# Optimization experiments

Measured on AMD Instinct MI355X. Metric: run time of the kernel, lower is better.

## Reference

```python
import jax, jax.numpy as jnp
import numpy as np

N = 128
NPTS = 120000
G = 64  # voxel grid side


def _build_coords_and_nbrs():
    rng = np.random.default_rng(0)
    lin = rng.choice(G ** 3, size=NPTS, replace=False)
    xs = lin // (G * G)
    ys = (lin // G) % G
    zs = lin % G
    lut = np.full(G ** 3, -1, np.int32)
    lut[lin] = np.arange(NPTS, dtype=np.int32)
    nbr = np.full((NPTS, 27), -1, np.int32)
    k = 0
    for dx in (-1, 0, 1):
        for dy in (-1, 0, 1):
            for dz in (-1, 0, 1):
                nx, ny, nz = xs + dx, ys + dy, zs + dz
                ok = (nx >= 0) & (nx < G) & (ny >= 0) & (ny < G) & (nz >= 0) & (nz < G)
                nl = np.clip(nx * G * G + ny * G + nz, 0, G ** 3 - 1)
                nbr[:, k] = np.where(ok, lut[nl], -1)
                k += 1
    return nbr


def setup_inputs() -> dict:
    key = jax.random.key(0)
    k = jax.random.split(key, 6)
    H = N // 2
    x = jax.random.normal(k[0], (NPTS, N), jnp.float32)
    W1s = jax.random.normal(k[1], (6, N, H), jnp.float32) * np.sqrt(2.0 / N)
    Wks = jax.random.normal(k[2], (6, 27, H, H), jnp.float32) * np.sqrt(2.0 / (27 * H))
    W2s = jax.random.normal(k[3], (6, H, N), jnp.float32) * np.sqrt(1.0 / H)
    Wf = jax.random.normal(k[4], (N, N), jnp.float32) * np.sqrt(1.0 / N)
    nbr_idx = jnp.asarray(_build_coords_and_nbrs())
    return {"x": x, "W1s": W1s, "Wks": Wks, "W2s": W2s, "Wf": Wf, "nbr_idx": nbr_idx}


def reference(x, W1s, Wks, W2s, Wf, nbr_idx):
    valid = nbr_idx >= 0                      # [NPTS, 27]
    safe = jnp.maximum(nbr_idx, 0)

    def conv3(h, Wk):
        # gather-matmul-scatter over the 27 coordinate offsets (as ME does)
        out = jnp.zeros((h.shape[0], Wk.shape[2]), h.dtype)
        for kk in range(27):
            g = jnp.where(valid[:, kk, None], h[safe[:, kk]], 0.0)
            out = out + g @ Wk[kk]
        return out

    def residual_unit(h, i):
        t = jax.nn.relu(h @ W1s[i])           # 1x1 conv N -> N/2
        t = jax.nn.relu(conv3(t, Wks[i]))     # 3^3 sparse conv N/2 -> N/2
        t = t @ W2s[i]                        # 1x1 conv N/2 -> N
        return jax.nn.relu(t + h)

    a = x
    for i in range(3):
        a = residual_unit(a, i)
    b = x
    for i in range(3, 6):
        b = residual_unit(b, i)
    b = b @ Wf                                # final 1x1 conv in branch b
    return a * jax.nn.sigmoid(b) + x
```

## Files before the change

### kernel.cpp

```cpp
#include <hip/hip_runtime.h>
#include <stdint.h>

#define NPTS 120000

typedef __attribute__((ext_vector_type(8))) short bf16x8;
typedef __attribute__((ext_vector_type(4))) float f32x4;

__device__ __forceinline__ uint16_t f2b(float f) {
    union { float f; uint32_t i; } v; v.f = f;
    uint32_t x = v.i;
    return (uint16_t)((x + 0x7fffu + ((x >> 16) & 1u)) >> 16);
}
__device__ __forceinline__ float b2f(uint16_t u) {
    union { uint32_t i; float f; } v; v.i = ((uint32_t)u) << 16; return v.f;
}
__device__ __forceinline__ bf16x8 cvt8(f32x4 a, f32x4 b) {
    bf16x8 t;
    t[0] = (short)f2b(a[0]); t[1] = (short)f2b(a[1]);
    t[2] = (short)f2b(a[2]); t[3] = (short)f2b(a[3]);
    t[4] = (short)f2b(b[0]); t[5] = (short)f2b(b[1]);
    t[6] = (short)f2b(b[2]); t[7] = (short)f2b(b[3]);
    return t;
}
#define MFMA(a, b, c) __builtin_amdgcn_mfma_f32_16x16x32_bf16((a), (b), (c), 0, 0, 0)

__global__ __launch_bounds__(256) void k_swz(
    const float* __restrict__ W1s, const float* __restrict__ Wks,
    const float* __restrict__ W2s, const float* __restrict__ Wf,
    uint16_t* __restrict__ Z, uint16_t* __restrict__ T1z,
    uint16_t* __restrict__ T2z)
{
    if (blockIdx.x == 0) {
        if (threadIdx.x < 64)
            T1z[(size_t)NPTS * 64 + threadIdx.x] = 0;
        else if (threadIdx.x < 128 && T2z)
            T2z[(size_t)NPTS * 64 + (threadIdx.x - 64)] = 0;
    }
    int idx = blockIdx.x * 256 + threadIdx.x;
    if (idx >= 778240) return;
    const float* src; int K, N, r;
    if (idx < 49152)       { src = W1s + (idx / 8192) * 8192;           K = 128; N = 64;  r = idx & 8191; }
    else if (idx < 712704) { int t = idx - 49152;  src = Wks + (t >> 12) * 4096; K = 64;  N = 64;  r = t & 4095; }
    else if (idx < 761856) { int t = idx - 712704; src = W2s + (t / 8192) * 8192; K = 64;  N = 128; r = t & 8191; }
    else                   { src = Wf; K = 128; N = 128; r = idx - 761856; }
    int j  = r & 7;
    int l  = (r >> 3) & 63;
    int t2 = r >> 9;
    int KC = K >> 5;
    int kc = t2 % KC;
    int nt = t2 / KC;
    int k  = kc * 32 + (l >> 4) * 8 + j;
    int n  = nt * 16 + (l & 15);
    Z[idx] = f2b(src[k * N + n]);
}

__global__ __launch_bounds__(256) void k_nbrT(
    const int* __restrict__ nbr, int* __restrict__ nbrT)
{
    __shared__ int st[27 * 64];
    const int tid = threadIdx.x;
    const long p0 = (long)blockIdx.x * 64;
    for (int i = tid; i < 1728; i += 256) {
        int lp = i / 27, kk = i - lp * 27;
        int n = nbr[p0 * 27 + i];
        st[kk * 64 + lp] = ((n < 0) ? NPTS : n) << 6;
    }
    __syncthreads();
    for (int i = tid; i < 1728; i += 256) {
        int kk = i >> 6, lp = i & 63;
        nbrT[(long)kk * NPTS + p0 + lp] = st[i];
    }
}

__device__ __forceinline__ void gemm1_body(
    int b, const float* __restrict__ H, const uint16_t* __restrict__ Wz,
    uint16_t* __restrict__ T)
{
    const int tid = threadIdx.x;
    const int wv = tid >> 6, ln = tid & 63;
    const int m = ln & 15, part = ln >> 4;
    const long rb = (long)b * 64 + wv * 16;

    bf16x8 a[4];
    const float* hrow = H + (rb + m) * 128 + part * 8;
    #pragma unroll
    for (int kc = 0; kc < 4; ++kc) {
        f32x4 h0 = *reinterpret_cast<const f32x4*>(hrow + kc * 32);
        f32x4 h1 = *reinterpret_cast<const f32x4*>(hrow + kc * 32 + 4);
        a[kc] = cvt8(h0, h1);
    }
    #pragma unroll
    for (int nt = 0; nt < 4; ++nt) {
        f32x4 acc = (f32x4)(0.0f);
        #pragma unroll
        for (int kc = 0; kc < 4; ++kc) {
            bf16x8 b8 = *reinterpret_cast<const bf16x8*>(Wz + ((nt * 4 + kc) * 64 + ln) * 8);
            acc = MFMA(a[kc], b8, acc);
        }
        #pragma unroll
        for (int r = 0; r < 4; ++r) {
            float v = acc[r] > 0.f ? acc[r] : 0.f;
            T[(rb + part * 4 + r) * 64 + nt * 16 + m] = f2b(v);
        }
    }
}

__global__ __launch_bounds__(256) void k_gemm1(
    const float* __restrict__ H, const uint16_t* __restrict__ Wz,
    uint16_t* __restrict__ T)
{
    gemm1_body(blockIdx.x, H, Wz, T);
}

__global__ __launch_bounds__(256) void k_gemm1p(
    const float* __restrict__ HA, const float* __restrict__ HB,
    const uint16_t* __restrict__ WzA, const uint16_t* __restrict__ WzB,
    uint16_t* __restrict__ TA, uint16_t* __restrict__ TB)
{
    int b = blockIdx.x;
    if (b < 1875) gemm1_body(b, HA, WzA, TA);
    else          gemm1_body(b - 1875, HB, WzB, TB);
}

struct SM {
    uint16_t wkbuf[2][4096];
    uint16_t uni[4][3456];
};

__device__ __forceinline__ void gather6(bf16x8 (&dst)[3][2], const int (&ix)[3],
                                        const uint16_t* __restrict__ T, int pc8)
{
    #pragma unroll
    for (int mm = 0; mm < 3; ++mm) {
        const uint16_t* s = T + (long)ix[mm] + pc8;
        dst[mm][0] = *reinterpret_cast<const bf16x8*>(s);
        dst[mm][1] = *reinterpret_cast<const bf16x8*>(s + 32);
    }
}
__device__ __forceinline__ void ldidx(int (&ix)[3], const int* __restrict__ p, int mrow)
{
    #pragma unroll
    for (int mm = 0; mm < 3; ++mm) ix[mm] = p[mm * 16 + mrow];
}
__device__ __forceinline__ void pload(bf16x8& s0, bf16x8& s1, const uint16_t* __restrict__ g)
{
    s0 = *reinterpret_cast<const bf16x8*>(g);
    s1 = *reinterpret_cast<const bf16x8*>(g + 512);
}
__device__ __forceinline__ void tap24(f32x4 (&acc)[3][4], const bf16x8 (&A)[3][2],
                                      const uint16_t* wk, int ln)
{
    bf16x8 B[8];
    #pragma unroll
    for (int i = 0; i < 8; ++i)
        B[i] = *reinterpret_cast<const bf16x8*>(wk + i * 512 + ln * 8);
    #pragma unroll
    for (int nt = 0; nt < 4; ++nt)
        #pragma unroll
        for (int mm = 0; mm < 3; ++mm) {
            acc[mm][nt] = MFMA(A[mm][0], B[nt * 2 + 0], acc[mm][nt]);
            acc[mm][nt] = MFMA(A[mm][1], B[nt * 2 + 1], acc[mm][nt]);
        }
}

template<int MODE>
__device__ __forceinline__ void conv_body(
    SM& sm, int blk,
    const uint16_t* __restrict__ T, const uint16_t* __restrict__ Wkz,
    const uint16_t* __restrict__ W2z, const float* Hin,
    const int* __restrict__ nbrT, float* HoutF, uint16_t* __restrict__ HoutB)
{
    const int tid = threadIdx.x;
    const int wv = tid >> 6, ln = tid & 63;
    const int mrow = ln & 15, part = ln >> 4, pc8 = part * 8;
    const long bb = (long)blk * 192;
    const long wb0 = bb + wv * 48;

    {
        bf16x8 s0, s1;
        pload(s0, s1, Wkz + wv * 1024 + ln * 8);
        *reinterpret_cast<bf16x8*>(&sm.wkbuf[0][wv * 1024 + ln * 8]) = s0;
        *reinterpret_cast<bf16x8*>(&sm.wkbuf[0][wv * 1024 + 512 + ln * 8]) = s1;
    }
    int ixA[3], ixB[3];
    bf16x8 pA[3][2], pB[3][2];
    ldidx(ixA, nbrT + wb0, mrow);
    gather6(pA, ixA, T, pc8);
    ldidx(ixB, nbrT + (long)NPTS + wb0, mrow);

    f32x4 acc[3][4];
    #pragma unroll
    for (int mm = 0; mm < 3; ++mm)
        #pragma unroll
        for (int nt = 0; nt < 4; ++nt) acc[mm][nt] = (f32x4)(0.0f);
    __syncthreads();

    #pragma unroll 1
    for (int t = 0; t < 26; t += 2) {
        bf16x8 s0, s1;
        gather6(pB, ixB, T, pc8);
        pload(s0, s1, Wkz + (t + 1) * 4096 + wv * 1024 + ln * 8);
        if (t + 2 < 27) ldidx(ixA, nbrT + (long)(t + 2) * NPTS + wb0, mrow);
        tap24(acc, pA, &sm.wkbuf[0][0], ln);
        *reinterpret_cast<bf16x8*>(&sm.wkbuf[1][wv * 1024 + ln * 8]) = s0;
        *reinterpret_cast<bf16x8*>(&sm.wkbuf[1][wv * 1024 + 512 + ln * 8]) = s1;
        __syncthreads();
        if (t + 1 < 26) {
            gather6(pA, ixA, T, pc8);
            pload(s0, s1, Wkz + (t + 2) * 4096 + wv * 1024 + ln * 8);
            if (t + 3 < 27) ldidx(ixB, nbrT + (long)(t + 3) * NPTS + wb0, mrow);
        }
        tap24(acc, pB, &sm.wkbuf[1][0], ln);
        if (t + 1 < 26) {
            *reinterpret_cast<bf16x8*>(&sm.wkbuf[0][wv * 1024 + ln * 8]) = s0;
            *reinterpret_cast<bf16x8*>(&sm.wkbuf[0][wv * 1024 + 512 + ln * 8]) = s1;
        }
        __syncthreads();
    }
    tap24(acc, pA, &sm.wkbuf[0][0], ln);

    uint16_t* sc2 = &sm.uni[wv][0];
    #pragma unroll
    for (int mm = 0; mm < 3; ++mm)
        #pragma unroll
        for (int nt = 0; nt < 4; ++nt)
            #pragma unroll
            for (int r = 0; r < 4; ++r) {
                float v = acc[mm][nt][r];
                v = v > 0.f ? v : 0.f;
                sc2[(mm * 16 + part * 4 + r) * 72 + nt * 16 + mrow] = f2b(v);
            }
    __builtin_amdgcn_wave_barrier();

    bf16x8 a2[3][2];
    #pragma unroll
    for (int mm = 0; mm < 3; ++mm) {
        const uint16_t* crow = sc2 + (mm * 16 + mrow) * 72;
        a2[mm][0] = *reinterpret_cast<const bf16x8*>(crow + pc8);
        a2[mm][1] = *reinterpret_cast<const bf16x8*>(crow + 32 + pc8);
    }
    __builtin_amdgcn_wave_barrier();

    #pragma unroll 2
    for (int nt = 0; nt < 8; ++nt) {
        bf16x8 b0 = *reinterpret_cast<const bf16x8*>(W2z + ((nt * 2 + 0) * 64 + ln) * 8);
        bf16x8 b1 = *reinterpret_cast<const bf16x8*>(W2z + ((nt * 2 + 1) * 64 + ln) * 8);
        f32x4 c[3];
        #pragma unroll
        for (int mm = 0; mm < 3; ++mm) {
            c[mm] = (f32x4)(0.0f);
            c[mm] = MFMA(a2[mm][0], b0, c[mm]);
            c[mm] = MFMA(a2[mm][1], b1, c[mm]);
        }
        const int col = nt * 16 + mrow;
        if (MODE == 0) {
            #pragma unroll
            for (int mm = 0; mm < 3; ++mm)
                #pragma unroll
                for (int r = 0; r < 4; ++r) {
                    long p = wb0 + mm * 16 + part * 4 + r;
                    float v = c[mm][r] + Hin[p * 128 + col];
                    HoutF[p * 128 + col] = v > 0.f ? v : 0.f;
                }
        } else {
            #pragma unroll
            for (int mm = 0; mm < 3; ++mm)
                #pragma unroll
                for (int r = 0; r < 4; ++r) {
                    long p = wb0 + mm * 16 + part * 4 + r;
                    float v = c[mm][r] + Hin[p * 128 + col];
                    v = v > 0.f ? v : 0.f;
                    HoutB[p * 128 + col] = f2b(v);
                }
        }
    }
}

template<int MODE>
__global__ __launch_bounds__(256, 3) void k_conv1(
    const uint16_t* __restrict__ T, const uint16_t* __restrict__ Wkz,
    const uint16_t* __restrict__ W2z, const float* Hin,
    const int* __restrict__ nbrT, float* HoutF, uint16_t* __restrict__ HoutB)
{
    __shared__ SM sm;
    conv_body<MODE>(sm, blockIdx.x, T, Wkz, W2z, Hin, nbrT, HoutF, HoutB);
}

template<int MA, int MB>
__global__ __launch_bounds__(256, 3) void k_convp(
    const uint16_t* __restrict__ Ta, const uint16_t* __restrict__ Tb,
    const uint16_t* __restrict__ WkzA, const uint16_t* __restrict__ WkzB,
    const uint16_t* __restrict__ W2zA, const uint16_t* __restrict__ W2zB,
    const float* HinA, const float* HinB,
    const int* __restrict__ nbrT,
    float* HoFA, float* HoFB,
    uint16_t* __restrict__ HoBA, uint16_t* __restrict__ HoBB)
{
    __shared__ SM sm;
    int b = blockIdx.x;
    if (b < 625) conv_body<MA>(sm, b, Ta, WkzA, W2zA, HinA, nbrT, HoFA, HoBA);
    else         conv_body<MB>(sm, b - 625, Tb, WkzB, W2zB, HinB, nbrT, HoFB, HoBB);
}

__global__ __launch_bounds__(256) void k_final(
    const float* B, const uint16_t* __restrict__ Wfz,
    const uint16_t* __restrict__ A16, const float* __restrict__ X,
    float* Out)
{
    const int tid = threadIdx.x;
    const int wv = tid >> 6, ln = tid & 63;
    const int m = ln & 15, part = ln >> 4;
    const long rb = (long)blockIdx.x * 64 + wv * 16;

    bf16x8 a[4];
    const float* brow = B + (rb + m) * 128 + part * 8;
    #pragma unroll
    for (int kc = 0; kc < 4; ++kc) {
        f32x4 h0 = *reinterpret_cast<const f32x4*>(brow + kc * 32);
        f32x4 h1 = *reinterpret_cast<const f32x4*>(brow + kc * 32 + 4);
        a[kc] = cvt8(h0, h1);
    }
    #pragma unroll
    for (int nt = 0; nt < 8; ++nt) {
        f32x4 acc = (f32x4)(0.0f);
        #pragma unroll
        for (int kc = 0; kc < 4; ++kc) {
            bf16x8 b = *reinterpret_cast<const bf16x8*>(Wfz + ((nt * 4 + kc) * 64 + ln) * 8);
            acc = MFMA(a[kc], b, acc);
        }
        #pragma unroll
        for (int r = 0; r < 4; ++r) {
            long p = rb + part * 4 + r;
            int col = nt * 16 + m;
            float s = 1.f / (1.f + __expf(-acc[r]));
            float av = b2f(A16[p * 128 + col]);
            Out[p * 128 + col] = av * s + X[p * 128 + col];
        }
    }
}

extern "C" void kernel_launch(void* const* d_in, const int* in_sizes, int n_in,
                              void* d_out, int out_size, void* d_ws, size_t ws_size,
                              hipStream_t stream)
{
    const float* x   = (const float*)d_in[0];
    const float* W1s = (const float*)d_in[1];
    const float* Wks = (const float*)d_in[2];
    const float* W2s = (const float*)d_in[3];
    const float* Wf  = (const float*)d_in[4];
    const int*   nbr = (const int*)d_in[5];
    float*       out = (float*)d_out;

    const size_t A16_sh = (size_t)NPTS * 128;
    const size_t T_sh   = (size_t)(NPTS + 1) * 64;
    const size_t Z_sh   = 778240;
    const size_t nbrT_i = (size_t)27 * NPTS;

    uint16_t* A16 = (uint16_t*)d_ws;
    uint16_t* Ta  = A16 + A16_sh;
    uint16_t* Tb  = Ta + T_sh;
    uint16_t* Z   = Tb + T_sh;
    int* nbrT     = (int*)(Z + Z_sh);
    float* Ha     = (float*)(nbrT + nbrT_i);
    size_t need_paired = (size_t)((char*)(Ha + A16_sh) - (char*)d_ws);

    if (ws_size >= need_paired) {
        const uint16_t* W1z = Z;
        const uint16_t* Wkz = Z + 49152;
        const uint16_t* W2z = Z + 712704;
        const uint16_t* Wfz = Z + 761856;

        k_swz <<<dim3(3040), dim3(256), 0, stream>>>(W1s, Wks, W2s, Wf, Z, Ta, Tb);
        k_nbrT<<<dim3(1875), dim3(256), 0, stream>>>(nbr, nbrT);

        k_gemm1p<<<dim3(3750), dim3(256), 0, stream>>>(x, x, W1z, W1z + 3 * 8192, Ta, Tb);
        k_convp<0, 0><<<dim3(1250), dim3(256), 0, stream>>>(
            Ta, Tb, Wkz + 0 * 110592, Wkz + 3 * 110592, W2z + 0 * 8192, W2z + 3 * 8192,
            x, x, nbrT, Ha, out, nullptr, nullptr);
        k_gemm1p<<<dim3(3750), dim3(256), 0, stream>>>(Ha, out, W1z + 1 * 8192, W1z + 4 * 8192, Ta, Tb);
        k_convp<0, 0><<<dim3(1250), dim3(256), 0, stream>>>(
            Ta, Tb, Wkz + 1 * 110592, Wkz + 4 * 110592, W2z + 1 * 8192, W2z + 4 * 8192,
            Ha, out, nbrT, Ha, out, nullptr, nullptr);
        k_gemm1p<<<dim3(3750), dim3(256), 0, stream>>>(Ha, out, W1z + 2 * 8192, W1z + 5 * 8192, Ta, Tb);
        k_convp<1, 0><<<dim3(1250), dim3(256), 0, stream>>>(
            Ta, Tb, Wkz + 2 * 110592, Wkz + 5 * 110592, W2z + 2 * 8192, W2z + 5 * 8192,
            Ha, out, nbrT, nullptr, out, A16, nullptr);
        k_final<<<dim3(1875), dim3(256), 0, stream>>>(out, Wfz, A16, x, out);
    } else {
        uint16_t* Zs   = Ta + T_sh;
        int* nbrTs     = (int*)(Zs + Z_sh);
        const uint16_t* W1z = Zs;
        const uint16_t* Wkz = Zs + 49152;
        const uint16_t* W2z = Zs + 712704;
        const uint16_t* Wfz = Zs + 761856;

        k_swz <<<dim3(3040), dim3(256), 0, stream>>>(W1s, Wks, W2s, Wf, Zs, Ta, nullptr);
        k_nbrT<<<dim3(1875), dim3(256), 0, stream>>>(nbr, nbrTs);

        auto g1 = [&](int i, const float* h) {
            k_gemm1<<<dim3(1875), dim3(256), 0, stream>>>(h, W1z + (size_t)i * 8192, Ta);
        };
        g1(0, x);
        k_conv1<0><<<dim3(625), dim3(256), 0, stream>>>(Ta, Wkz + 0 * 110592, W2z + 0 * 8192, x,   nbrTs, out, nullptr);
        g1(1, out);
        k_conv1<0><<<dim3(625), dim3(256), 0, stream>>>(Ta, Wkz + 1 * 110592, W2z + 1 * 8192, out, nbrTs, out, nullptr);
        g1(2, out);
        k_conv1<1><<<dim3(625), dim3(256), 0, stream>>>(Ta, Wkz + 2 * 110592, W2z + 2 * 8192, out, nbrTs, nullptr, A16);
        g1(3, x);
        k_conv1<0><<<dim3(625), dim3(256), 0, stream>>>(Ta, Wkz + 3 * 110592, W2z + 3 * 8192, x,   nbrTs, out, nullptr);
        g1(4, out);
        k_conv1<0><<<dim3(625), dim3(256), 0, stream>>>(Ta, Wkz + 4 * 110592, W2z + 4 * 8192, out, nbrTs, out, nullptr);
        g1(5, out);
        k_conv1<0><<<dim3(625), dim3(256), 0, stream>>>(Ta, Wkz + 5 * 110592, W2z + 5 * 8192, out, nbrTs, out, nullptr);
        k_final<<<dim3(1875), dim3(256), 0, stream>>>(out, Wfz, A16, x, out);
    }
}
```

Measured before the change: 666.8 us.

## Use single-wave conv blocks reading tap weights directly from global memory

```diff
diff --git a/kernel.cpp b/kernel.cpp
--- a/kernel.cpp
+++ b/kernel.cpp
@@ -122,11 +122,6 @@
     else          gemm1_body(b - 1875, HB, WzB, TB);
 }
 
-struct SM {
-    uint16_t wkbuf[2][4096];
-    uint16_t uni[4][3456];
-};
-
 __device__ __forceinline__ void gather6(bf16x8 (&dst)[3][2], const int (&ix)[3],
                                         const uint16_t* __restrict__ T, int pc8)
 {
@@ -142,18 +137,13 @@
     #pragma unroll
     for (int mm = 0; mm < 3; ++mm) ix[mm] = p[mm * 16 + mrow];
 }
-__device__ __forceinline__ void pload(bf16x8& s0, bf16x8& s1, const uint16_t* __restrict__ g)
-{
-    s0 = *reinterpret_cast<const bf16x8*>(g);
-    s1 = *reinterpret_cast<const bf16x8*>(g + 512);
-}
-__device__ __forceinline__ void tap24(f32x4 (&acc)[3][4], const bf16x8 (&A)[3][2],
-                                      const uint16_t* wk, int ln)
+__device__ __forceinline__ void tap24g(f32x4 (&acc)[3][4], const bf16x8 (&A)[3][2],
+                                       const uint16_t* __restrict__ wk, int ln)
 {
     bf16x8 B[8];
     #pragma unroll
     for (int i = 0; i < 8; ++i)
-        B[i] = *reinterpret_cast<const bf16x8*>(wk + i * 512 + ln * 8);
+        B[i] = *reinterpret_cast<const bf16x8*>(wk + (i * 64 + ln) * 8);
     #pragma unroll
     for (int nt = 0; nt < 4; ++nt)
         #pragma unroll
@@ -164,24 +154,16 @@
 }
 
 template<int MODE>
-__device__ __forceinline__ void conv_body(
-    SM& sm, int blk,
+__device__ __forceinline__ void conv_body1(
+    uint16_t* sc2, int blk,
     const uint16_t* __restrict__ T, const uint16_t* __restrict__ Wkz,
     const uint16_t* __restrict__ W2z, const float* Hin,
     const int* __restrict__ nbrT, float* HoutF, uint16_t* __restrict__ HoutB)
 {
-    const int tid = threadIdx.x;
-    const int wv = tid >> 6, ln = tid & 63;
+    const int ln = threadIdx.x & 63;
     const int mrow = ln & 15, part = ln >> 4, pc8 = part * 8;
-    const long bb = (long)blk * 192;
-    const long wb0 = bb + wv * 48;
-
-    {
-        bf16x8 s0, s1;
-        pload(s0, s1, Wkz + wv * 1024 + ln * 8);
-        *reinterpret_cast<bf16x8*>(&sm.wkbuf[0][wv * 1024 + ln * 8]) = s0;
-        *reinterpret_cast<bf16x8*>(&sm.wkbuf[0][wv * 1024 + 512 + ln * 8]) = s1;
-    }
+    const long wb0 = (long)blk * 48;
+
     int ixA[3], ixB[3];
     bf16x8 pA[3][2], pB[3][2];
     ldidx(ixA, nbrT + wb0, mrow);
@@ -193,33 +175,20 @@
     for (int mm = 0; mm < 3; ++mm)
         #pragma unroll
         for (int nt = 0; nt < 4; ++nt) acc[mm][nt] = (f32x4)(0.0f);
-    __syncthreads();
 
     #pragma unroll 1
     for (int t = 0; t < 26; t += 2) {
-        bf16x8 s0, s1;
         gather6(pB, ixB, T, pc8);
-        pload(s0, s1, Wkz + (t + 1) * 4096 + wv * 1024 + ln * 8);
         if (t + 2 < 27) ldidx(ixA, nbrT + (long)(t + 2) * NPTS + wb0, mrow);
-        tap24(acc, pA, &sm.wkbuf[0][0], ln);
-        *reinterpret_cast<bf16x8*>(&sm.wkbuf[1][wv * 1024 + ln * 8]) = s0;
-        *reinterpret_cast<bf16x8*>(&sm.wkbuf[1][wv * 1024 + 512 + ln * 8]) = s1;
-        __syncthreads();
+        tap24g(acc, pA, Wkz + t * 4096, ln);
         if (t + 1 < 26) {
             gather6(pA, ixA, T, pc8);
-            pload(s0, s1, Wkz + (t + 2) * 4096 + wv * 1024 + ln * 8);
             if (t + 3 < 27) ldidx(ixB, nbrT + (long)(t + 3) * NPTS + wb0, mrow);
         }
-        tap24(acc, pB, &sm.wkbuf[1][0], ln);
-        if (t + 1 < 26) {
-            *reinterpret_cast<bf16x8*>(&sm.wkbuf[0][wv * 1024 + ln * 8]) = s0;
-            *reinterpret_cast<bf16x8*>(&sm.wkbuf[0][wv * 1024 + 512 + ln * 8]) = s1;
-        }
-        __syncthreads();
-    }
-    tap24(acc, pA, &sm.wkbuf[0][0], ln);
-
-    uint16_t* sc2 = &sm.uni[wv][0];
+        tap24g(acc, pB, Wkz + (t + 1) * 4096, ln);
+    }
+    tap24g(acc, pA, Wkz + 26 * 4096, ln);
+
     #pragma unroll
     for (int mm = 0; mm < 3; ++mm)
         #pragma unroll
@@ -277,17 +246,17 @@
 }
 
 template<int MODE>
-__global__ __launch_bounds__(256, 3) void k_conv1(
+__global__ __launch_bounds__(64, 4) void k_conv1(
     const uint16_t* __restrict__ T, const uint16_t* __restrict__ Wkz,
     const uint16_t* __restrict__ W2z, const float* Hin,
     const int* __restrict__ nbrT, float* HoutF, uint16_t* __restrict__ HoutB)
 {
-    __shared__ SM sm;
-    conv_body<MODE>(sm, blockIdx.x, T, Wkz, W2z, Hin, nbrT, HoutF, HoutB);
+    __shared__ uint16_t sc2[48 * 72];
+    conv_body1<MODE>(sc2, blockIdx.x, T, Wkz, W2z, Hin, nbrT, HoutF, HoutB);
 }
 
 template<int MA, int MB>
-__global__ __launch_bounds__(256, 3) void k_convp(
+__global__ __launch_bounds__(64, 4) void k_convp1(
     const uint16_t* __restrict__ Ta, const uint16_t* __restrict__ Tb,
     const uint16_t* __restrict__ WkzA, const uint16_t* __restrict__ WkzB,
     const uint16_t* __restrict__ W2zA, const uint16_t* __restrict__ W2zB,
@@ -296,10 +265,10 @@
     float* HoFA, float* HoFB,
     uint16_t* __restrict__ HoBA, uint16_t* __restrict__ HoBB)
 {
-    __shared__ SM sm;
+    __shared__ uint16_t sc2[48 * 72];
     int b = blockIdx.x;
-    if (b < 625) conv_body<MA>(sm, b, Ta, WkzA, W2zA, HinA, nbrT, HoFA, HoBA);
-    else         conv_body<MB>(sm, b - 625, Tb, WkzB, W2zB, HinB, nbrT, HoFB, HoBB);
+    if (b < 2500) conv_body1<MA>(sc2, b, Ta, WkzA, W2zA, HinA, nbrT, HoFA, HoBA);
+    else          conv_body1<MB>(sc2, b - 2500, Tb, WkzB, W2zB, HinB, nbrT, HoFB, HoBB);
 }
 
 __global__ __launch_bounds__(256) void k_final(
@@ -374,15 +343,15 @@
         k_nbrT<<<dim3(1875), dim3(256), 0, stream>>>(nbr, nbrT);
 
         k_gemm1p<<<dim3(3750), dim3(256), 0, stream>>>(x, x, W1z, W1z + 3 * 8192, Ta, Tb);
-        k_convp<0, 0><<<dim3(1250), dim3(256), 0, stream>>>(
+        k_convp1<0, 0><<<dim3(5000), dim3(64), 0, stream>>>(
             Ta, Tb, Wkz + 0 * 110592, Wkz + 3 * 110592, W2z + 0 * 8192, W2z + 3 * 8192,
             x, x, nbrT, Ha, out, nullptr, nullptr);
         k_gemm1p<<<dim3(3750), dim3(256), 0, stream>>>(Ha, out, W1z + 1 * 8192, W1z + 4 * 8192, Ta, Tb);
-        k_convp<0, 0><<<dim3(1250), dim3(256), 0, stream>>>(
+        k_convp1<0, 0><<<dim3(5000), dim3(64), 0, stream>>>(
             Ta, Tb, Wkz + 1 * 110592, Wkz + 4 * 110592, W2z + 1 * 8192, W2z + 4 * 8192,
             Ha, out, nbrT, Ha, out, nullptr, nullptr);
         k_gemm1p<<<dim3(3750), dim3(256), 0, stream>>>(Ha, out, W1z + 2 * 8192, W1z + 5 * 8192, Ta, Tb);
-        k_convp<1, 0><<<dim3(1250), dim3(256), 0, stream>>>(
+        k_convp1<1, 0><<<dim3(5000), dim3(64), 0, stream>>>(
             Ta, Tb, Wkz + 2 * 110592, Wkz + 5 * 110592, W2z + 2 * 8192, W2z + 5 * 8192,
             Ha, out, nbrT, nullptr, out, A16, nullptr);
         k_final<<<dim3(1875), dim3(256), 0, stream>>>(out, Wfz, A16, x, out);
@@ -401,17 +370,17 @@
             k_gemm1<<<dim3(1875), dim3(256), 0, stream>>>(h, W1z + (size_t)i * 8192, Ta);
         };
         g1(0, x);
-        k_conv1<0><<<dim3(625), dim3(256), 0, stream>>>(Ta, Wkz + 0 * 110592, W2z + 0 * 8192, x,   nbrTs, out, nullptr);
+        k_conv1<0><<<dim3(2500), dim3(64), 0, stream>>>(Ta, Wkz + 0 * 110592, W2z + 0 * 8192, x,   nbrTs, out, nullptr);
         g1(1, out);
-        k_conv1<0><<<dim3(625), dim3(256), 0, stream>>>(Ta, Wkz + 1 * 110592, W2z + 1 * 8192, out, nbrTs, out, nullptr);
+        k_conv1<0><<<dim3(2500), dim3(64), 0, stream>>>(Ta, Wkz + 1 * 110592, W2z + 1 * 8192, out, nbrTs, out, nullptr);
         g1(2, out);
-        k_conv1<1><<<dim3(625), dim3(256), 0, stream>>>(Ta, Wkz + 2 * 110592, W2z + 2 * 8192, out, nbrTs, nullptr, A16);
+        k_conv1<1><<<dim3(2500), dim3(64), 0, stream>>>(Ta, Wkz + 2 * 110592, W2z + 2 * 8192, out, nbrTs, nullptr, A16);
         g1(3, x);
-        k_conv1<0><<<dim3(625), dim3(256), 0, stream>>>(Ta, Wkz + 3 * 110592, W2z + 3 * 8192, x,   nbrTs, out, nullptr);
+        k_conv1<0><<<dim3(2500), dim3(64), 0, stream>>>(Ta, Wkz + 3 * 110592, W2z + 3 * 8192, x,   nbrTs, out, nullptr);
         g1(4, out);
-        k_conv1<0><<<dim3(625), dim3(256), 0, stream>>>(Ta, Wkz + 4 * 110592, W2z + 4 * 8192, out, nbrTs, out, nullptr);
+        k_conv1<0><<<dim3(2500), dim3(64), 0, stream>>>(Ta, Wkz + 4 * 110592, W2z + 4 * 8192, out, nbrTs, out, nullptr);
         g1(5, out);
-        k_conv1<0><<<dim3(625), dim3(256), 0, stream>>>(Ta, Wkz + 5 * 110592, W2z + 5 * 8192, out, nbrTs, out, nullptr);
+        k_conv1<0><<<dim3(2500), dim3(64), 0, stream>>>(Ta, Wkz + 5 * 110592, W2z + 5 * 8192, out, nbrTs, out, nullptr);
         k_final<<<dim3(1875), dim3(256), 0, stream>>>(out, Wfz, A16, x, out);
     }
 }
```

Result: slower. 777.6 us (+16.6%).

## Stage MFMA epilogues through LDS for coalesced vector global stores

Applied to the files above, without the earlier changes.

```diff
diff --git a/kernel.cpp b/kernel.cpp
--- a/kernel.cpp
+++ b/kernel.cpp
@@ -5,6 +5,7 @@
 
 typedef __attribute__((ext_vector_type(8))) short bf16x8;
 typedef __attribute__((ext_vector_type(4))) float f32x4;
+typedef __attribute__((ext_vector_type(4))) unsigned short u16x4;
 
 __device__ __forceinline__ uint16_t f2b(float f) {
     union { float f; uint32_t i; } v; v.f = f;
@@ -73,13 +74,14 @@
 }
 
 __device__ __forceinline__ void gemm1_body(
-    int b, const float* __restrict__ H, const uint16_t* __restrict__ Wz,
-    uint16_t* __restrict__ T)
+    uint16_t* ts, int b, const float* __restrict__ H,
+    const uint16_t* __restrict__ Wz, uint16_t* __restrict__ T)
 {
     const int tid = threadIdx.x;
     const int wv = tid >> 6, ln = tid & 63;
     const int m = ln & 15, part = ln >> 4;
     const long rb = (long)b * 64 + wv * 16;
+    uint16_t* myts = ts + wv * 1024;
 
     bf16x8 a[4];
     const float* hrow = H + (rb + m) * 128 + part * 8;
@@ -100,8 +102,16 @@
         #pragma unroll
         for (int r = 0; r < 4; ++r) {
             float v = acc[r] > 0.f ? acc[r] : 0.f;
-            T[(rb + part * 4 + r) * 64 + nt * 16 + m] = f2b(v);
-        }
+            myts[(part * 4 + r) * 64 + nt * 16 + m] = f2b(v);
+        }
+    }
+    __builtin_amdgcn_wave_barrier();
+    #pragma unroll
+    for (int it = 0; it < 4; ++it) {
+        int idx = it * 256 + ln * 4;
+        int row = idx >> 6, col = idx & 63;
+        *reinterpret_cast<u16x4*>(&T[(rb + row) * 64 + col]) =
+            *reinterpret_cast<const u16x4*>(&myts[idx]);
     }
 }
 
@@ -109,7 +119,8 @@
     const float* __restrict__ H, const uint16_t* __restrict__ Wz,
     uint16_t* __restrict__ T)
 {
-    gemm1_body(blockIdx.x, H, Wz, T);
+    __shared__ uint16_t ts[4 * 1024];
+    gemm1_body(ts, blockIdx.x, H, Wz, T);
 }
 
 __global__ __launch_bounds__(256) void k_gemm1p(
@@ -117,15 +128,11 @@
     const uint16_t* __restrict__ WzA, const uint16_t* __restrict__ WzB,
     uint16_t* __restrict__ TA, uint16_t* __restrict__ TB)
 {
+    __shared__ uint16_t ts[4 * 1024];
     int b = blockIdx.x;
-    if (b < 1875) gemm1_body(b, HA, WzA, TA);
-    else          gemm1_body(b - 1875, HB, WzB, TB);
-}
-
-struct SM {
-    uint16_t wkbuf[2][4096];
-    uint16_t uni[4][3456];
-};
+    if (b < 1875) gemm1_body(ts, b, HA, WzA, TA);
+    else          gemm1_body(ts, b - 1875, HB, WzB, TB);
+}
 
 __device__ __forceinline__ void gather6(bf16x8 (&dst)[3][2], const int (&ix)[3],
                                         const uint16_t* __restrict__ T, int pc8)
@@ -165,7 +172,7 @@
 
 template<int MODE>
 __device__ __forceinline__ void conv_body(
-    SM& sm, int blk,
+    char* smem, int blk,
     const uint16_t* __restrict__ T, const uint16_t* __restrict__ Wkz,
     const uint16_t* __restrict__ W2z, const float* Hin,
     const int* __restrict__ nbrT, float* HoutF, uint16_t* __restrict__ HoutB)
@@ -176,11 +183,14 @@
     const long bb = (long)blk * 192;
     const long wb0 = bb + wv * 48;
 
+    uint16_t* wk0 = (uint16_t*)smem;
+    uint16_t* wk1 = (uint16_t*)(smem + 8192);
+
     {
         bf16x8 s0, s1;
         pload(s0, s1, Wkz + wv * 1024 + ln * 8);
-        *reinterpret_cast<bf16x8*>(&sm.wkbuf[0][wv * 1024 + ln * 8]) = s0;
-        *reinterpret_cast<bf16x8*>(&sm.wkbuf[0][wv * 1024 + 512 + ln * 8]) = s1;
+        *reinterpret_cast<bf16x8*>(&wk0[wv * 1024 + ln * 8]) = s0;
+        *reinterpret_cast<bf16x8*>(&wk0[wv * 1024 + 512 + ln * 8]) = s1;
     }
     int ixA[3], ixB[3];
     bf16x8 pA[3][2], pB[3][2];
@@ -201,25 +211,28 @@
         gather6(pB, ixB, T, pc8);
         pload(s0, s1, Wkz + (t + 1) * 4096 + wv * 1024 + ln * 8);
         if (t + 2 < 27) ldidx(ixA, nbrT + (long)(t + 2) * NPTS + wb0, mrow);
-        tap24(acc, pA, &sm.wkbuf[0][0], ln);
-        *reinterpret_cast<bf16x8*>(&sm.wkbuf[1][wv * 1024 + ln * 8]) = s0;
-        *reinterpret_cast<bf16x8*>(&sm.wkbuf[1][wv * 1024 + 512 + ln * 8]) = s1;
+        tap24(acc, pA, wk0, ln);
+        *reinterpret_cast<bf16x8*>(&wk1[wv * 1024 + ln * 8]) = s0;
+        *reinterpret_cast<bf16x8*>(&wk1[wv * 1024 + 512 + ln * 8]) = s1;
         __syncthreads();
         if (t + 1 < 26) {
             gather6(pA, ixA, T, pc8);
             pload(s0, s1, Wkz + (t + 2) * 4096 + wv * 1024 + ln * 8);
             if (t + 3 < 27) ldidx(ixB, nbrT + (long)(t + 3) * NPTS + wb0, mrow);
         }
-        tap24(acc, pB, &sm.wkbuf[1][0], ln);
+        tap24(acc, pB, wk1, ln);
         if (t + 1 < 26) {
-            *reinterpret_cast<bf16x8*>(&sm.wkbuf[0][wv * 1024 + ln * 8]) = s0;
-            *reinterpret_cast<bf16x8*>(&sm.wkbuf[0][wv * 1024 + 512 + ln * 8]) = s1;
+            *reinterpret_cast<bf16x8*>(&wk0[wv * 1024 + ln * 8]) = s0;
+            *reinterpret_cast<bf16x8*>(&wk0[wv * 1024 + 512 + ln * 8]) = s1;
         }
         __syncthreads();
     }
-    tap24(acc, pA, &sm.wkbuf[0][0], ln);
-
-    uint16_t* sc2 = &sm.uni[wv][0];
+    tap24(acc, pA, wk0, ln);
+    __syncthreads();
+
+    char* myr = smem + wv * 8192;
+    uint16_t* sc2 = (uint16_t*)myr;
+
     #pragma unroll
     for (int mm = 0; mm < 3; ++mm)
         #pragma unroll
@@ -241,53 +254,63 @@
     }
     __builtin_amdgcn_wave_barrier();
 
-    #pragma unroll 2
-    for (int nt = 0; nt < 8; ++nt) {
-        bf16x8 b0 = *reinterpret_cast<const bf16x8*>(W2z + ((nt * 2 + 0) * 64 + ln) * 8);
-        bf16x8 b1 = *reinterpret_cast<const bf16x8*>(W2z + ((nt * 2 + 1) * 64 + ln) * 8);
-        f32x4 c[3];
-        #pragma unroll
-        for (int mm = 0; mm < 3; ++mm) {
-            c[mm] = (f32x4)(0.0f);
-            c[mm] = MFMA(a2[mm][0], b0, c[mm]);
-            c[mm] = MFMA(a2[mm][1], b1, c[mm]);
-        }
-        const int col = nt * 16 + mrow;
-        if (MODE == 0) {
+    float* stg = (float*)myr;
+    #pragma unroll 1
+    for (int mm = 0; mm < 3; ++mm) {
+        #pragma unroll 2
+        for (int nt = 0; nt < 8; ++nt) {
+            bf16x8 b0 = *reinterpret_cast<const bf16x8*>(W2z + ((nt * 2 + 0) * 64 + ln) * 8);
+            bf16x8 b1 = *reinterpret_cast<const bf16x8*>(W2z + ((nt * 2 + 1) * 64 + ln) * 8);
+            f32x4 c = (f32x4)(0.0f);
+            c = MFMA(a2[mm][0], b0, c);
+            c = MFMA(a2[mm][1], b1, c);
             #pragma unroll
-            for (int mm = 0; mm < 3; ++mm)
+            for (int r = 0; r < 4; ++r)
+                stg[(part * 4 + r) * 128 + nt * 16 + mrow] = c[r];
+        }
+        __builtin_amdgcn_wave_barrier();
+        #pragma unroll
+        for (int it = 0; it < 8; ++it) {
+            int idx = it * 256 + ln * 4;
+            int row = idx >> 7, col = idx & 127;
+            long p = wb0 + mm * 16 + row;
+            f32x4 s = *reinterpret_cast<const f32x4*>(&stg[idx]);
+            f32x4 h = *reinterpret_cast<const f32x4*>(&Hin[p * 128 + col]);
+            if (MODE == 0) {
+                f32x4 o;
                 #pragma unroll
-                for (int r = 0; r < 4; ++r) {
-                    long p = wb0 + mm * 16 + part * 4 + r;
-                    float v = c[mm][r] + Hin[p * 128 + col];
-                    HoutF[p * 128 + col] = v > 0.f ? v : 0.f;
+                for (int q = 0; q < 4; ++q) {
+                    float v = s[q] + h[q];
+                    o[q] = v > 0.f ? v : 0.f;
                 }
-        } else {
-            #pragma unroll
-            for (int mm = 0; mm < 3; ++mm)
+                *reinterpret_cast<f32x4*>(&HoutF[p * 128 + col]) = o;
+            } else {
+                u16x4 o;
                 #pragma unroll
-                for (int r = 0; r < 4; ++r) {
-                    long p = wb0 + mm * 16 + part * 4 + r;
-                    float v = c[mm][r] + Hin[p * 128 + col];
+                for (int q = 0; q < 4; ++q) {
+                    float v = s[q] + h[q];
                     v = v > 0.f ? v : 0.f;
-                    HoutB[p * 128 + col] = f2b(v);
+                    o[q] = f2b(v);
                 }
-        }
+                *reinterpret_cast<u16x4*>(&HoutB[p * 128 + col]) = o;
+            }
+        }
+        __builtin_amdgcn_wave_barrier();
     }
 }
 
 template<int MODE>
-__global__ __launch_bounds__(256, 3) void k_conv1(
+__global__ __launch_bounds__(256, 5) void k_conv1(
     const uint16_t* __restrict__ T, const uint16_t* __restrict__ Wkz,
     const uint16_t* __restrict__ W2z, const float* Hin,
     const int* __restrict__ nbrT, float* HoutF, uint16_t* __restrict__ HoutB)
 {
-    __shared__ SM sm;
-    conv_body<MODE>(sm, blockIdx.x, T, Wkz, W2z, Hin, nbrT, HoutF, HoutB);
+    __shared__ __align__(16) char smem[32768];
+    conv_body<MODE>(smem, blockIdx.x, T, Wkz, W2z, Hin, nbrT, HoutF, HoutB);
 }
 
 template<int MA, int MB>
-__global__ __launch_bounds__(256, 3) void k_convp(
+__global__ __launch_bounds__(256, 5) void k_convp(
     const uint16_t* __restrict__ Ta, const uint16_t* __restrict__ Tb,
     const uint16_t* __restrict__ WkzA, const uint16_t* __restrict__ WkzB,
     const uint16_t* __restrict__ W2zA, const uint16_t* __restrict__ W2zB,
@@ -296,10 +319,10 @@
     float* HoFA, float* HoFB,
     uint16_t* __restrict__ HoBA, uint16_t* __restrict__ HoBB)
 {
-    __shared__ SM sm;
+    __shared__ __align__(16) char smem[32768];
     int b = blockIdx.x;
-    if (b < 625) conv_body<MA>(sm, b, Ta, WkzA, W2zA, HinA, nbrT, HoFA, HoBA);
-    else         conv_body<MB>(sm, b - 625, Tb, WkzB, W2zB, HinB, nbrT, HoFB, HoBB);
+    if (b < 625) conv_body<MA>(smem, b, Ta, WkzA, W2zA, HinA, nbrT, HoFA, HoBA);
+    else         conv_body<MB>(smem, b - 625, Tb, WkzB, W2zB, HinB, nbrT, HoFB, HoBB);
 }
 
 __global__ __launch_bounds__(256) void k_final(
@@ -307,6 +330,7 @@
     const uint16_t* __restrict__ A16, const float* __restrict__ X,
     float* Out)
 {
+    __shared__ __align__(16) float fs[4][2048];
     const int tid = threadIdx.x;
     const int wv = tid >> 6, ln = tid & 63;
     const int m = ln & 15, part = ln >> 4;
@@ -329,13 +353,25 @@
             acc = MFMA(a[kc], b, acc);
         }
         #pragma unroll
-        for (int r = 0; r < 4; ++r) {
-            long p = rb + part * 4 + r;
-            int col = nt * 16 + m;
-            float s = 1.f / (1.f + __expf(-acc[r]));
-            float av = b2f(A16[p * 128 + col]);
-            Out[p * 128 + col] = av * s + X[p * 128 + col];
-        }
+        for (int r = 0; r < 4; ++r)
+            fs[wv][(part * 4 + r) * 128 + nt * 16 + m] = acc[r];
+    }
+    __builtin_amdgcn_wave_barrier();
+    #pragma unroll
+    for (int it = 0; it < 8; ++it) {
+        int idx = it * 256 + ln * 4;
+        int row = idx >> 7, col = idx & 127;
+        long p = rb + row;
+        f32x4 t = *reinterpret_cast<const f32x4*>(&fs[wv][idx]);
+        u16x4 av = *reinterpret_cast<const u16x4*>(&A16[p * 128 + col]);
+        f32x4 xx = *reinterpret_cast<const f32x4*>(&X[p * 128 + col]);
+        f32x4 o;
+        #pragma unroll
+        for (int q = 0; q < 4; ++q) {
+            float s = 1.f / (1.f + __expf(-t[q]));
+            o[q] = b2f(av[q]) * s + xx[q];
+        }
+        *reinterpret_cast<f32x4*>(&Out[p * 128 + col]) = o;
     }
 }
 
```

Result: slower. 955.9 us (+43.4%).
